# Performance work log

Hardware: AMD Instinct MI355X
Metric: run time of the kernel (lower is better)

Reference implementation:

```python
import jax, jax.numpy as jnp
import numpy as np

N, DEG, F_IN, F_OUT = 50000, 16, 128, 128
E = N * DEG


def setup_inputs() -> dict:
    key = jax.random.key(0)
    k1, k2, k3 = jax.random.split(key, 3)
    x = jax.random.normal(k1, (N, F_IN), dtype=jnp.float32)
    # flat ragged neighbor features: edge e belongs to node seg_ids[e]
    neigh = jax.random.normal(k2, (E, F_IN), dtype=jnp.float32)
    seg_ids = (jnp.arange(E, dtype=jnp.int32) // DEG)  # sorted, each node has DEG neighbors
    # nn.Linear(in, out, bias=False) weight: [out_features, in_features]
    W = jax.random.normal(k3, (F_OUT, F_IN), dtype=jnp.float32) / np.sqrt(F_IN)
    return {"x": x, "neigh": neigh, "seg_ids": seg_ids, "W": W}


def reference(x, neigh, seg_ids, W):
    n = x.shape[0]
    # per-node mean of neighbor features (segment mean over ragged lists)
    ones = jnp.ones((neigh.shape[0],), dtype=x.dtype)
    counts = jax.ops.segment_sum(ones, seg_ids, num_segments=n)  # [N]
    f = jax.ops.segment_sum(neigh, seg_ids, num_segments=n) / counts[:, None]  # [N, F_in]
    # shared linear transform (no bias)
    x_out = (x + f) @ W.T          # [N, F_out]
    neigh_out = neigh @ W.T        # [E, F_out] (all ragged neighbor sets, flat)
    return (x_out, neigh_out)
```

## Files before the change

kernel.cpp:

```cpp
#include <hip/hip_runtime.h>
#include <hip/hip_bf16.h>

#define FDIM  128
#define GNODE 8
#define DEGC  16
#define TROWS 128
#define ROWB  256
#define WIMG  (FDIM * ROWB)

typedef __attribute__((ext_vector_type(8))) short   bvec8;
typedef __attribute__((ext_vector_type(8))) __bf16  bf16v8;
typedef __attribute__((ext_vector_type(4))) float   fvec4;

__device__ __forceinline__ fvec4 mfma16(bvec8 a, bvec8 b, fvec4 c) {
    return __builtin_amdgcn_mfma_f32_16x16x32_bf16(
        __builtin_bit_cast(bf16v8, a), __builtin_bit_cast(bf16v8, b), c, 0, 0, 0);
}

__device__ __forceinline__ bvec8 ld8(const char* base, int row, int bir) {
    return *(const bvec8*)(base + row * ROWB + (bir ^ ((row & 7) << 4)));
}

__device__ __forceinline__ bvec8 cvt8(fvec4 lo, fvec4 hi) {
    bf16v8 o;
    o[0] = (__bf16)lo.x; o[1] = (__bf16)lo.y; o[2] = (__bf16)lo.z; o[3] = (__bf16)lo.w;
    o[4] = (__bf16)hi.x; o[5] = (__bf16)hi.y; o[6] = (__bf16)hi.z; o[7] = (__bf16)hi.w;
    return __builtin_bit_cast(bvec8, o);
}

__device__ __forceinline__ bvec8 ldcvt(const float* __restrict__ p) {
    return cvt8(((const fvec4*)p)[0], ((const fvec4*)p)[1]);
}

__global__ void prep_w(const float* __restrict__ W, char* __restrict__ wimg) {
    const int u   = blockIdx.x * 256 + threadIdx.x;
    const int row = u >> 4, sl = u & 15;
    bvec8 o = ldcvt(W + (size_t)row * FDIM + sl * 8);
    *(bvec8*)(wimg + row * ROWB + ((sl * 16) ^ ((row & 7) << 4))) = o;
}

__global__ __launch_bounds__(256, 3)
void gcn_fused(const float* __restrict__ x, const float* __restrict__ neigh,
               const char* __restrict__ wimg,
               float* __restrict__ out_x, float* __restrict__ out_nb)
{
    __shared__ __align__(16) char lds_w[WIMG];

    const int t    = threadIdx.x;
    const int blk  = blockIdx.x;
    const int wave = t >> 6, lane = t & 63;
    const int lr = lane & 15, lg = lane >> 4;

    #pragma unroll
    for (int i = 0; i < 8; ++i) {
        const int off = wave * 1024 + i * 4096 + lane * 16;
        __builtin_amdgcn_global_load_lds((const unsigned int*)(wimg + off),
                                         (unsigned int*)(lds_w + off), 16, 0, 0);
    }

    const float* arow0 = neigh + ((size_t)blk * TROWS + wave * 32 + lr) * FDIM;
    const float* arow1 = arow0 + 16 * FDIM;
    fvec4 af0[8], af1[8];
    #pragma unroll
    for (int q = 0; q < 8; ++q) {
        const int idx = (q >> 1) * 8 + lg * 2 + (q & 1);
        af0[q] = ((const fvec4*)arow0)[idx];
        af1[q] = ((const fvec4*)arow1)[idx];
    }

    const float* xrow = x + ((size_t)(blk * GNODE) + wave * 2 + (lr & 1)) * FDIM;
    fvec4 xf[8];
    #pragma unroll
    for (int q = 0; q < 8; ++q)
        xf[q] = ((const fvec4*)xrow)[(q >> 1) * 8 + lg * 2 + (q & 1)];

    __syncthreads();

    bvec8 a0f[4], a1f[4], axf[4];
    #pragma unroll
    for (int ks = 0; ks < 4; ++ks) {
        a0f[ks] = cvt8(af0[ks * 2], af0[ks * 2 + 1]);
        a1f[ks] = cvt8(af1[ks * 2], af1[ks * 2 + 1]);
        axf[ks] = cvt8(xf[ks * 2],  xf[ks * 2 + 1]);
    }

    fvec4 acc[2][8];
    #pragma unroll
    for (int i = 0; i < 2; ++i)
        #pragma unroll
        for (int j = 0; j < 8; ++j) acc[i][j] = (fvec4){0.f, 0.f, 0.f, 0.f};

    #pragma unroll
    for (int ks = 0; ks < 4; ++ks) {
        const int kb = ks * 64 + lg * 16;
        #pragma unroll
        for (int tn = 0; tn < 8; ++tn) {
            bvec8 b = ld8(lds_w, tn * 16 + lr, kb);
            acc[0][tn] = mfma16(a0f[ks], b, acc[0][tn]);
            acc[1][tn] = mfma16(a1f[ks], b, acc[1][tn]);
        }
    }

    #pragma unroll
    for (int tm = 0; tm < 2; ++tm) {
        const size_t rbase = (size_t)blk * TROWS + wave * 32 + tm * 16 + lg * 4;
        #pragma unroll
        for (int tn = 0; tn < 8; ++tn)
            #pragma unroll
            for (int r = 0; r < 4; ++r)
                out_nb[(rbase + r) * FDIM + tn * 16 + lr] = acc[tm][tn][r];
    }

    float p[2][8];
    #pragma unroll
    for (int tm = 0; tm < 2; ++tm)
        #pragma unroll
        for (int tn = 0; tn < 8; ++tn) {
            float s = acc[tm][tn][0] + acc[tm][tn][1] + acc[tm][tn][2] + acc[tm][tn][3];
            s += __shfl_xor(s, 16);
            s += __shfl_xor(s, 32);
            p[tm][tn] = s * (1.f / 16.f);
        }

    fvec4 accx[8];
    #pragma unroll
    for (int j = 0; j < 8; ++j) accx[j] = (fvec4){0.f, 0.f, 0.f, 0.f};
    #pragma unroll
    for (int ks = 0; ks < 4; ++ks) {
        const int kb = ks * 64 + lg * 16;
        #pragma unroll
        for (int tn = 0; tn < 8; ++tn) {
            bvec8 b = ld8(lds_w, tn * 16 + lr, kb);
            accx[tn] = mfma16(axf[ks], b, accx[tn]);
        }
    }

    if (lg == 0) {
        #pragma unroll
        for (int r = 0; r < 2; ++r) {
            const size_t node = (size_t)blk * GNODE + wave * 2 + r;
            #pragma unroll
            for (int tn = 0; tn < 8; ++tn)
                out_x[node * FDIM + tn * 16 + lr] = accx[tn][r] + p[r][tn];
        }
    }
}

extern "C" void kernel_launch(void* const* d_in, const int* in_sizes, int n_in,
                              void* d_out, int out_size, void* d_ws, size_t ws_size,
                              hipStream_t stream) {
    const float* x     = (const float*)d_in[0];
    const float* neigh = (const float*)d_in[1];
    const float* W     = (const float*)d_in[3];

    const int n = in_sizes[0] / FDIM;
    float* out_x  = (float*)d_out;
    float* out_nb = out_x + (size_t)n * FDIM;
    char*  wimg   = (char*)d_ws;

    hipLaunchKernelGGL(prep_w, dim3(8), dim3(256), 0, stream, W, wimg);

    const int blocks = n / GNODE;
    hipLaunchKernelGGL(gcn_fused, dim3(blocks), dim3(256), 0, stream,
                       x, neigh, wimg, out_x, out_nb);
}
```

Measured before the change: 170.0 us.

## Use 512-thread blocks with one node per wave instead of two

Doubles the block to 8 waves so each wave handles 16 neighbor rows (one node) instead of 32, halving per-wave accumulator registers and raising resident waves per CU. The LDS weight load is spread across 8 waves, and the x-row MFMA now uses a single broadcast row per wave. The extra waves give more memory-level parallelism for this bandwidth-bound kernel, at the cost of fewer loads in flight per wave and a heavier block-wide barrier.

New measurement: 168.3 us, median of 2. Within noise of the previous version (-1.0%).

```diff
diff --git a/kernel.cpp b/kernel.cpp
--- a/kernel.cpp
+++ b/kernel.cpp
@@ -39,7 +39,7 @@
     *(bvec8*)(wimg + row * ROWB + ((sl * 16) ^ ((row & 7) << 4))) = o;
 }
 
-__global__ __launch_bounds__(256, 3)
+__global__ __launch_bounds__(512, 4)
 void gcn_fused(const float* __restrict__ x, const float* __restrict__ neigh,
                const char* __restrict__ wimg,
                float* __restrict__ out_x, float* __restrict__ out_nb)
@@ -52,23 +52,19 @@
     const int lr = lane & 15, lg = lane >> 4;
 
     #pragma unroll
-    for (int i = 0; i < 8; ++i) {
-        const int off = wave * 1024 + i * 4096 + lane * 16;
+    for (int i = 0; i < 4; ++i) {
+        const int off = i * 8192 + wave * 1024 + lane * 16;
         __builtin_amdgcn_global_load_lds((const unsigned int*)(wimg + off),
                                          (unsigned int*)(lds_w + off), 16, 0, 0);
     }
 
-    const float* arow0 = neigh + ((size_t)blk * TROWS + wave * 32 + lr) * FDIM;
-    const float* arow1 = arow0 + 16 * FDIM;
-    fvec4 af0[8], af1[8];
+    const float* arow = neigh + ((size_t)blk * TROWS + wave * 16 + lr) * FDIM;
+    fvec4 af[8];
     #pragma unroll
-    for (int q = 0; q < 8; ++q) {
-        const int idx = (q >> 1) * 8 + lg * 2 + (q & 1);
-        af0[q] = ((const fvec4*)arow0)[idx];
-        af1[q] = ((const fvec4*)arow1)[idx];
-    }
+    for (int q = 0; q < 8; ++q)
+        af[q] = ((const fvec4*)arow)[(q >> 1) * 8 + lg * 2 + (q & 1)];
 
-    const float* xrow = x + ((size_t)(blk * GNODE) + wave * 2 + (lr & 1)) * FDIM;
+    const float* xrow = x + ((size_t)(blk * GNODE) + wave) * FDIM;
     fvec4 xf[8];
     #pragma unroll
     for (int q = 0; q < 8; ++q)
@@ -76,19 +72,16 @@
 
     __syncthreads();
 
-    bvec8 a0f[4], a1f[4], axf[4];
+    bvec8 afr[4], axf[4];
     #pragma unroll
     for (int ks = 0; ks < 4; ++ks) {
-        a0f[ks] = cvt8(af0[ks * 2], af0[ks * 2 + 1]);
-        a1f[ks] = cvt8(af1[ks * 2], af1[ks * 2 + 1]);
-        axf[ks] = cvt8(xf[ks * 2],  xf[ks * 2 + 1]);
+        afr[ks] = cvt8(af[ks * 2], af[ks * 2 + 1]);
+        axf[ks] = cvt8(xf[ks * 2], xf[ks * 2 + 1]);
     }
 
-    fvec4 acc[2][8];
+    fvec4 acc[8];
     #pragma unroll
-    for (int i = 0; i < 2; ++i)
-        #pragma unroll
-        for (int j = 0; j < 8; ++j) acc[i][j] = (fvec4){0.f, 0.f, 0.f, 0.f};
+    for (int j = 0; j < 8; ++j) acc[j] = (fvec4){0.f, 0.f, 0.f, 0.f};
 
     #pragma unroll
     for (int ks = 0; ks < 4; ++ks) {
@@ -96,31 +89,25 @@
         #pragma unroll
         for (int tn = 0; tn < 8; ++tn) {
             bvec8 b = ld8(lds_w, tn * 16 + lr, kb);
-            acc[0][tn] = mfma16(a0f[ks], b, acc[0][tn]);
-            acc[1][tn] = mfma16(a1f[ks], b, acc[1][tn]);
+            acc[tn] = mfma16(afr[ks], b, acc[tn]);
         }
     }
 
+    const size_t rbase = (size_t)blk * TROWS + wave * 16 + lg * 4;
     #pragma unroll
-    for (int tm = 0; tm < 2; ++tm) {
-        const size_t rbase = (size_t)blk * TROWS + wave * 32 + tm * 16 + lg * 4;
+    for (int tn = 0; tn < 8; ++tn)
         #pragma unroll
-        for (int tn = 0; tn < 8; ++tn)
-            #pragma unroll
-            for (int r = 0; r < 4; ++r)
-                out_nb[(rbase + r) * FDIM + tn * 16 + lr] = acc[tm][tn][r];
+        for (int r = 0; r < 4; ++r)
+            out_nb[(rbase + r) * FDIM + tn * 16 + lr] = acc[tn][r];
+
+    float p[8];
+    #pragma unroll
+    for (int tn = 0; tn < 8; ++tn) {
+        float s = acc[tn][0] + acc[tn][1] + acc[tn][2] + acc[tn][3];
+        s += __shfl_xor(s, 16);
+        s += __shfl_xor(s, 32);
+        p[tn] = s * (1.f / 16.f);
     }
-
-    float p[2][8];
-    #pragma unroll
-    for (int tm = 0; tm < 2; ++tm)
-        #pragma unroll
-        for (int tn = 0; tn < 8; ++tn) {
-            float s = acc[tm][tn][0] + acc[tm][tn][1] + acc[tm][tn][2] + acc[tm][tn][3];
-            s += __shfl_xor(s, 16);
-            s += __shfl_xor(s, 32);
-            p[tm][tn] = s * (1.f / 16.f);
-        }
 
     fvec4 accx[8];
     #pragma unroll
@@ -136,13 +123,10 @@
     }
 
     if (lg == 0) {
+        const size_t node = (size_t)blk * GNODE + wave;
         #pragma unroll
-        for (int r = 0; r < 2; ++r) {
-            const size_t node = (size_t)blk * GNODE + wave * 2 + r;
-            #pragma unroll
-            for (int tn = 0; tn < 8; ++tn)
-                out_x[node * FDIM + tn * 16 + lr] = accx[tn][r] + p[r][tn];
-        }
+        for (int tn = 0; tn < 8; ++tn)
+            out_x[node * FDIM + tn * 16 + lr] = accx[tn][0] + p[tn];
     }
 }
 
@@ -161,6 +145,6 @@
     hipLaunchKernelGGL(prep_w, dim3(8), dim3(256), 0, stream, W, wimg);
 
     const int blocks = n / GNODE;
-    hipLaunchKernelGGL(gcn_fused, dim3(blocks), dim3(256), 0, stream,
+    hipLaunchKernelGGL(gcn_fused, dim3(blocks), dim3(512), 0, stream,
                        x, neigh, wimg, out_x, out_nb);
 }
```
